# Kernel optimization log

Hardware: AMD Instinct MI355X
Metric: run time of the kernel (lower is better)

The kernel has to match this reference:

```python
import jax, jax.numpy as jnp
import numpy as np

DIM = 768
HEADS = 12
HEAD_DIM = DIM // HEADS
RANK = 8
SCALING = 1.0 / RANK  # lora_alpha / r
SCALE = HEAD_DIM ** -0.5


def setup_inputs() -> dict:
    key = jax.random.key(0)
    ks = jax.random.split(key, 14)
    B, N, D, r = 4, 1024, DIM, RANK
    s = lambda k, shape, sd=0.02: jax.random.normal(k, shape, jnp.float32) * sd
    return {
        "x": jax.random.normal(ks[0], (B, N, D), jnp.float32),
        "qkv_w": s(ks[1], (3 * D, D)),
        "qkv_b": s(ks[2], (3 * D,)),
        "q_base_w": s(ks[3], (D, D)),
        "q_base_b": s(ks[4], (D,)),
        "q_A": s(ks[5], (r, D), 1.0 / r),
        "q_B": s(ks[6], (D, r)),
        "k_base_w": s(ks[7], (D, D)),
        "k_base_b": s(ks[8], (D,)),
        "k_A": s(ks[9], (r, D), 1.0 / r),
        "k_B": s(ks[10], (D, r)),
        "proj_w": s(ks[11], (D, D)),
        "proj_b": s(ks[12], (D,)),
    }


def _lora_linear(x, w, b, A, Bm):
    # base linear + LoRA delta: x@w.T + b + (x@A.T)@B.T * scaling
    return x @ w.T + b + ((x @ A.T) @ Bm.T) * SCALING


def reference(x, qkv_w, qkv_b, q_base_w, q_base_b, q_A, q_B,
              k_base_w, k_base_b, k_A, k_B, proj_w, proj_b):
    B, N, D = x.shape
    H, hd = HEADS, HEAD_DIM
    qkv = (x @ qkv_w.T + qkv_b).reshape(B, N, 3, H, hd).transpose(2, 0, 3, 1, 4)
    q, k, v = qkv[0], qkv[1], qkv[2]  # [B,H,N,hd]
    q_delta = _lora_linear(x, q_base_w, q_base_b, q_A, q_B).reshape(B, N, H, hd).transpose(0, 2, 1, 3)
    k_delta = _lora_linear(x, k_base_w, k_base_b, k_A, k_B).reshape(B, N, H, hd).transpose(0, 2, 1, 3)
    q = q + q_delta
    k = k + k_delta
    attn = jnp.einsum('bhnd,bhmd->bhnm', q, k) * SCALE
    attn = jax.nn.softmax(attn, axis=-1)
    out = jnp.einsum('bhnm,bhmd->bhnd', attn, v)
    out = out.transpose(0, 2, 1, 3).reshape(B, N, D)
    return out @ proj_w.T + proj_b
```

## Files before the change

kernel.cpp:

```cpp
#include <hip/hip_runtime.h>
#include <hip/hip_bf16.h>


typedef _Float16 half8 __attribute__((ext_vector_type(8)));
typedef float f32x4 __attribute__((ext_vector_type(4)));

typedef __attribute__((address_space(3))) unsigned int lds_u32;
typedef __attribute__((address_space(1))) const unsigned int glob_u32;

__device__ __forceinline__ void glds16(const void* g, void* l) {
    __builtin_amdgcn_global_load_lds((glob_u32*)g, (lds_u32*)l, 16, 0, 0);
}

__device__ __forceinline__ float pk2f16(float a, float b) {
    return __builtin_bit_cast(float, __builtin_amdgcn_cvt_pkrtz(a, b));
}

#define SMSCALE 0.18033688011112042f

constexpr size_t OFF_WX = 0;
constexpr size_t OFF_PH = OFF_WX + (size_t)2304*800*2;
constexpr size_t OFF_XE = OFF_PH + (size_t)768*768*2;
constexpr size_t OFF_QH = OFF_XE + (size_t)4096*800*2;
constexpr size_t OFF_KH = OFF_QH + (size_t)48*1024*64*2;
constexpr size_t OFF_VT = OFF_KH + (size_t)48*1024*64*2;
constexpr size_t OFF_AO = OFF_VT + (size_t)48*1024*64*2;

__global__ __launch_bounds__(256)
void pre(const float* __restrict__ qkv_w, const float* __restrict__ qkv_b,
         const float* __restrict__ qw, const float* __restrict__ qbias,
         const float* __restrict__ kw, const float* __restrict__ kbias,
         const float* __restrict__ proj_w, const float* __restrict__ qB,
         const float* __restrict__ kB, const float* __restrict__ x,
         const float* __restrict__ qA, const float* __restrict__ kA,
         _Float16* __restrict__ Wx, _Float16* __restrict__ Ph,
         _Float16* __restrict__ Xe) {
    const int t = threadIdx.x, bb = blockIdx.x;
    if (bb < 2304) {
        const int n = bb;
        const float rs = (n < 768) ? SMSCALE : 1.0f;
        const float* wsrc = qkv_w + (size_t)n * 768;
        const float* fold = (n < 768) ? (qw + (size_t)n * 768)
                          : (n < 1536 ? (kw + (size_t)(n - 768) * 768) : nullptr);
        _Float16* dst = Wx + (size_t)n * 800;
#pragma unroll
        for (int i = 0; i < 3; ++i) {
            const int c = t + i * 256;
            float v = wsrc[c];
            if (fold) v += fold[c];
            dst[c] = (_Float16)(v * rs);
        }
        if (t < 32) {
            float v = 0.f;
            if (t < 8)       { if (n < 768) v = rs * 0.125f * qB[n * 8 + t]; }
            else if (t < 16) { if (n >= 768 && n < 1536) v = 0.125f * kB[(size_t)(n - 768) * 8 + (t - 8)]; }
            else if (t == 16) v = rs * (qkv_b[n] + (n < 768 ? qbias[n] : (n < 1536 ? kbias[n - 768] : 0.f)));
            dst[768 + t] = (_Float16)v;
        }
    } else if (bb < 2880) {
        const size_t idx = ((size_t)(bb - 2304) * 256 + t) * 4;
        const float4 v = *(const float4*)(proj_w + idx);
        _Float16* d = Ph + idx;
        d[0] = (_Float16)v.x; d[1] = (_Float16)v.y;
        d[2] = (_Float16)v.z; d[3] = (_Float16)v.w;
    } else {
        __shared__ float xs[8][768];
        const int m0 = (bb - 2880) * 8;
#pragma unroll
        for (int i = t * 4; i < 6144; i += 1024) {
            const int r = i / 768, c = i - r * 768;
            const float4 v = *(const float4*)(x + (size_t)(m0 + r) * 768 + c);
            xs[r][c] = v.x; xs[r][c + 1] = v.y; xs[r][c + 2] = v.z; xs[r][c + 3] = v.w;
            _Float16* d = Xe + (size_t)(m0 + r) * 800 + c;
            d[0] = (_Float16)v.x; d[1] = (_Float16)v.y; d[2] = (_Float16)v.z; d[3] = (_Float16)v.w;
        }
        __syncthreads();

        const int j = t >> 4, lane = t & 15;
        const float* Arow = (j < 8) ? (qA + (size_t)j * 768) : (kA + (size_t)(j - 8) * 768);
        float accs[8] = {0.f, 0.f, 0.f, 0.f, 0.f, 0.f, 0.f, 0.f};
        for (int k = lane; k < 768; k += 16) {
            const float a = Arow[k];
#pragma unroll
            for (int r = 0; r < 8; ++r) accs[r] += xs[r][k] * a;
        }
#pragma unroll
        for (int r = 0; r < 8; ++r) {
            float acc = accs[r];
            acc += __shfl_xor(acc, 1); acc += __shfl_xor(acc, 2);
            acc += __shfl_xor(acc, 4); acc += __shfl_xor(acc, 8);
            if (lane == 0) Xe[(size_t)(m0 + r) * 800 + 768 + j] = (_Float16)acc;
        }
        if (t < 128) {
            const int r = t >> 4, c = t & 15;
            Xe[(size_t)(m0 + r) * 800 + 784 + c] = (c == 0) ? (_Float16)1.f : (_Float16)0.f;
        }
    }
}

template<int BM, int BN, int MODE>
__global__ __launch_bounds__(256)
void gemm_h(const _Float16* __restrict__ A, const _Float16* __restrict__ Bw,
            const int lda, const int ldb, const int nsteps,
            const float* __restrict__ bias,
            _Float16* __restrict__ Oq, _Float16* __restrict__ Ok, _Float16* __restrict__ Ov,
            float* __restrict__ Co) {
    constexpr int CA = BM / 16, CB = BN / 16, CT = CA + CB;
    constexpr int MI = BM / 32, NI = BN / 32;
    __shared__ __align__(16) _Float16 As[2][BM * 32];
    __shared__ __align__(16) _Float16 Bs[2][BN * 32];
    const int t = threadIdx.x;
    const int w = t >> 6, l = t & 63;
    const int l15 = l & 15, lg = l >> 4;
    const int wm = w >> 1, wn = w & 1;

    const int gx = gridDim.x;
    int lin = blockIdx.y * gx + blockIdx.x;
    lin = (lin & 7) * ((gx * gridDim.y) >> 3) + (lin >> 3);
    const int n0 = (lin % gx) * BN, m0 = (lin / gx) * BM;

    const _Float16* Abase = A + (size_t)(m0 + l15) * lda + lg * 8;
    const _Float16* Bbase = Bw + (size_t)(n0 + l15) * ldb + lg * 8;

    f32x4 acc[MI][NI];
#pragma unroll
    for (int mi = 0; mi < MI; ++mi)
#pragma unroll
        for (int ni = 0; ni < NI; ++ni) acc[mi][ni] = 0.f;

#pragma unroll
    for (int c = w; c < CT; c += 4) {
        if (c < CA) glds16(Abase + (size_t)(c * 16) * lda, &As[0][c * 512]);
        else        glds16(Bbase + (size_t)((c - CA) * 16) * ldb, &Bs[0][(c - CA) * 512]);
    }
    __syncthreads();

    for (int s = 0; s < nsteps; ++s) {
        const int cur = s & 1;
        if (s + 1 < nsteps) {
            const int ko = (s + 1) * 32;
#pragma unroll
            for (int c = w; c < CT; c += 4) {
                if (c < CA) glds16(Abase + (size_t)(c * 16) * lda + ko, &As[cur ^ 1][c * 512]);
                else        glds16(Bbase + (size_t)((c - CA) * 16) * ldb + ko, &Bs[cur ^ 1][(c - CA) * 512]);
            }
        }
        half8 a[MI], b[NI];
#pragma unroll
        for (int mi = 0; mi < MI; ++mi) a[mi] = *(const half8*)&As[cur][(wm * MI + mi) * 512 + l * 8];
#pragma unroll
        for (int ni = 0; ni < NI; ++ni) b[ni] = *(const half8*)&Bs[cur][(wn * NI + ni) * 512 + l * 8];
#pragma unroll
        for (int mi = 0; mi < MI; ++mi)
#pragma unroll
            for (int ni = 0; ni < NI; ++ni)
                acc[mi][ni] = __builtin_amdgcn_mfma_f32_16x16x32_f16(a[mi], b[ni], acc[mi][ni], 0, 0, 0);
        __syncthreads();
    }

    if (MODE == 0) {
        const int sel = (n0 >= 1536) ? 2 : (n0 >= 768 ? 1 : 0);
        const int b_ = m0 >> 10, nnb = m0 & 1023;
        if (sel < 2) {
            _Float16* dst = (sel == 0) ? Oq : Ok;
            const int jb = n0 - sel * 768;
#pragma unroll
            for (int mi = 0; mi < MI; ++mi)
#pragma unroll
                for (int reg = 0; reg < 4; ++reg) {
                    const int nn = nnb + wm * (BM / 2) + mi * 16 + lg * 4 + reg;
#pragma unroll
                    for (int ni = 0; ni < NI; ++ni) {
                        const int jj = jb + wn * (BN / 2) + ni * 16 + l15;
                        const int h = jj >> 6, d = jj & 63;
                        dst[(((size_t)(b_ * 12 + h)) * 1024 + nn) * 64 + d] = (_Float16)acc[mi][ni][reg];
                    }
                }
        } else {
#pragma unroll
            for (int mi = 0; mi < MI; ++mi) {
                const int nn = nnb + wm * (BM / 2) + mi * 16 + lg * 4;
#pragma unroll
                for (int ni = 0; ni < NI; ++ni) {
                    const int jj = (n0 - 1536) + wn * (BN / 2) + ni * 16 + l15;
                    const int h = jj >> 6, d = jj & 63;
                    float2 pv;
                    pv.x = pk2f16(acc[mi][ni][0], acc[mi][ni][1]);
                    pv.y = pk2f16(acc[mi][ni][2], acc[mi][ni][3]);
                    *(float2*)&Ov[(((size_t)(b_ * 12 + h)) * 64 + d) * 1024 + nn] = pv;
                }
            }
        }
    } else {
#pragma unroll
        for (int mi = 0; mi < MI; ++mi)
#pragma unroll
            for (int reg = 0; reg < 4; ++reg) {
                const int m = m0 + wm * (BM / 2) + mi * 16 + lg * 4 + reg;
#pragma unroll
                for (int ni = 0; ni < NI; ++ni) {
                    const int n = n0 + wn * (BN / 2) + ni * 16 + l15;
                    Co[(size_t)m * 768 + n] = acc[mi][ni][reg] + bias[n];
                }
            }
    }
}

#define STAGEK(kbt, buf) { \
_Pragma("unroll") \
    for (int i = 0; i < 4; ++i) { \
        const int c = w * 4 + i; \
        glds16(Kp + (size_t)((kbt) * 64 + (c >> 1) * 16 + l15) * 64 + (c & 1) * 32 + lg * 8, &Ks[buf][c * 512]); \
    } }
#define STAGEV(kbt, buf) { \
_Pragma("unroll") \
    for (int i = 0; i < 4; ++i) { \
        const int c = w * 4 + i; \
        glds16(Vp + (size_t)((c >> 1) * 16 + l15) * 1024 + (kbt) * 64 + (c & 1) * 32 + lg * 8, &Vs[buf][c * 512]); \
    } }
#define QK(buf, s) { \
    half8 kreg[8]; \
_Pragma("unroll") \
    for (int c = 0; c < 8; ++c) kreg[c] = *(const half8*)&Ks[buf][c * 512 + l * 8]; \
_Pragma("unroll") \
    for (int mi = 0; mi < 2; ++mi) \
_Pragma("unroll") \
        for (int nj = 0; nj < 4; ++nj) { \
            s[mi][nj] = 0.f; \
_Pragma("unroll") \
            for (int kh = 0; kh < 2; ++kh) \
                s[mi][nj] = __builtin_amdgcn_mfma_f32_16x16x32_f16(kreg[nj * 2 + kh], qf[mi][kh], s[mi][nj], 0, 0, 0); \
        } }
#define EXPP(ph, s) { \
_Pragma("unroll") \
    for (int mi = 0; mi < 2; ++mi) { \
        float ls = 0.f; \
_Pragma("unroll") \
        for (int nj = 0; nj < 4; ++nj) { \
            const float p0 = __builtin_amdgcn_exp2f(s[mi][nj][0]); \
            const float p1 = __builtin_amdgcn_exp2f(s[mi][nj][1]); \
            const float p2 = __builtin_amdgcn_exp2f(s[mi][nj][2]); \
            const float p3 = __builtin_amdgcn_exp2f(s[mi][nj][3]); \
            ls += (p0 + p1) + (p2 + p3); \
            float2 pk; \
            pk.x = pk2f16(p0, p1); \
            pk.y = pk2f16(p2, p3); \
            const int off = (mi * 2 + (nj >> 1)) * 512 + (2 * (nj & 1) + (lg >> 1)) * 128 \
                          + l15 * 8 + 4 * (lg & 1); \
            *(float2*)&Ps[w][ph][off] = pk; \
        } \
        lsum[mi] += ls; \
    } }
#define PV(ph, buf) { \
    half8 pf[2][2]; \
_Pragma("unroll") \
    for (int mi = 0; mi < 2; ++mi) \
_Pragma("unroll") \
        for (int kh = 0; kh < 2; ++kh) \
            pf[mi][kh] = *(const half8*)&Ps[w][ph][(mi * 2 + kh) * 512 + l * 8]; \
_Pragma("unroll") \
    for (int fj = 0; fj < 4; ++fj) \
_Pragma("unroll") \
        for (int kh = 0; kh < 2; ++kh) { \
            const half8 vf = *(const half8*)&Vs[buf][(fj * 2 + kh) * 512 + l * 8]; \
_Pragma("unroll") \
            for (int mi = 0; mi < 2; ++mi) \
                o[mi][fj] = __builtin_amdgcn_mfma_f32_16x16x32_f16(pf[mi][kh], vf, o[mi][fj], 0, 0, 0); \
        } }

__global__ __launch_bounds__(128)
void attn5(const _Float16* __restrict__ Q, const _Float16* __restrict__ K,
           const _Float16* __restrict__ Vt, _Float16* __restrict__ AO) {
    __shared__ __align__(16) _Float16 Ks[2][4096];
    __shared__ __align__(16) _Float16 Vs[2][4096];
    __shared__ __align__(16) _Float16 Ps[2][2][2048];
    __shared__ float sums[2][32];
    const int t = threadIdx.x;
    const int w = t >> 6, l = t & 63;
    const int l15 = l & 15, lg = l >> 4;

    int lin = blockIdx.y * 16 + blockIdx.x;
    lin = (lin & 7) * 96 + (lin >> 3);
    const int qb = lin & 15, bh = lin >> 4;

    const _Float16* Qp = Q  + (size_t)bh * 65536;
    const _Float16* Kp = K  + (size_t)bh * 65536;
    const _Float16* Vp = Vt + (size_t)bh * 65536;

    STAGEK(0, 0); STAGEK(1, 1); STAGEV(0, 0);
    half8 qf[2][2];
#pragma unroll
    for (int mi = 0; mi < 2; ++mi)
#pragma unroll
        for (int kh = 0; kh < 2; ++kh)
            qf[mi][kh] = *(const half8*)&Qp[(size_t)(qb * 64 + w * 32 + mi * 16 + l15) * 64 + kh * 32 + lg * 8];

    f32x4 o[2][4];
#pragma unroll
    for (int mi = 0; mi < 2; ++mi)
#pragma unroll
        for (int fj = 0; fj < 4; ++fj) o[mi][fj] = 0.f;
    float lsum[2] = {0.f, 0.f};
    __syncthreads();

    {
        f32x4 s[2][4];
        QK(0, s);
        EXPP(0, s);
    }
    __syncthreads();

    for (int kb = 0; kb < 15; ++kb) {
        const int cb = kb & 1, nb = cb ^ 1;
        if (kb + 2 < 16) STAGEK(kb + 2, cb);
        STAGEV(kb + 1, nb);
        f32x4 s[2][4];
        __builtin_amdgcn_s_setprio(1);
        QK(nb, s);
        PV(cb, cb);
        __builtin_amdgcn_s_setprio(0);
        EXPP(nb, s);
        __syncthreads();
    }
    PV(1, 1);

#pragma unroll
    for (int mi = 0; mi < 2; ++mi) {
        float tot = lsum[mi];
        tot += __shfl_xor(tot, 16);
        tot += __shfl_xor(tot, 32);
        if (lg == 0) sums[w][mi * 16 + l15] = tot;
    }
    __builtin_amdgcn_wave_barrier();

    const int b_ = bh / 12, h = bh % 12;
#pragma unroll
    for (int mi = 0; mi < 2; ++mi)
#pragma unroll
        for (int reg = 0; reg < 4; ++reg) {
            const float inv = 1.f / sums[w][mi * 16 + lg * 4 + reg];
            const int tok = qb * 64 + w * 32 + mi * 16 + lg * 4 + reg;
            const size_t base = ((size_t)(b_ * 1024 + tok)) * 768 + h * 64;
#pragma unroll
            for (int fj = 0; fj < 4; ++fj)
                AO[base + fj * 16 + l15] = (_Float16)(o[mi][fj][reg] * inv);
        }
}

extern "C" void kernel_launch(void* const* d_in, const int* in_sizes, int n_in,
                              void* d_out, int out_size, void* d_ws, size_t ws_size,
                              hipStream_t stream) {
    (void)in_sizes; (void)n_in; (void)out_size; (void)ws_size;
    const float* x      = (const float*)d_in[0];
    const float* qkv_w  = (const float*)d_in[1];
    const float* qkv_b  = (const float*)d_in[2];
    const float* q_bw   = (const float*)d_in[3];
    const float* q_bb   = (const float*)d_in[4];
    const float* q_A    = (const float*)d_in[5];
    const float* q_B    = (const float*)d_in[6];
    const float* k_bw   = (const float*)d_in[7];
    const float* k_bb   = (const float*)d_in[8];
    const float* k_A    = (const float*)d_in[9];
    const float* k_B    = (const float*)d_in[10];
    const float* proj_w = (const float*)d_in[11];
    const float* proj_b = (const float*)d_in[12];
    float* out = (float*)d_out;
    char*  ws  = (char*)d_ws;

    _Float16* Wx = (_Float16*)(ws + OFF_WX);
    _Float16* Ph = (_Float16*)(ws + OFF_PH);
    _Float16* Xe = (_Float16*)(ws + OFF_XE);
    _Float16* Qh = (_Float16*)(ws + OFF_QH);
    _Float16* Kh = (_Float16*)(ws + OFF_KH);
    _Float16* Vt = (_Float16*)(ws + OFF_VT);
    _Float16* AO = (_Float16*)(ws + OFF_AO);

    pre<<<dim3(3392), dim3(256), 0, stream>>>(qkv_w, qkv_b, q_bw, q_bb, k_bw, k_bb,
                                              proj_w, q_B, k_B, x, q_A, k_A, Wx, Ph, Xe);
    gemm_h<128, 96, 0><<<dim3(24, 32), dim3(256), 0, stream>>>(
        Xe, Wx, 800, 800, 25, nullptr, Qh, Kh, Vt, nullptr);
    attn5<<<dim3(16, 48), dim3(128), 0, stream>>>(Qh, Kh, Vt, AO);
    gemm_h<64, 96, 1><<<dim3(8, 64), dim3(256), 0, stream>>>(
        AO, Ph, 768, 768, 24, proj_b, nullptr, nullptr, nullptr, out);
}
```

Measured before the change: 99.67 us.

## Restructure attention loop to 128-key tiles with V loaded directly into registers

The attention kernel now processes 128 keys per iteration instead of 64, halving the loop count and the number of barriers. V fragments are read straight from global memory into registers rather than staged through LDS. The software pipeline that overlapped QK of the next tile with PV of the current one is dropped; K is double-buffered in LDS at twice the size. This trades cross-stage overlap and LDS reuse for fewer syncs and less LDS traffic, and it raises register pressure, which the launch bound of one block accepts.

```diff
diff --git a/kernel.cpp b/kernel.cpp
--- a/kernel.cpp
+++ b/kernel.cpp
@@ -206,74 +206,18 @@
     }
 }
 
-#define STAGEK(kbt, buf) { \
+#define STAGEK7(kbt, buf) { \
 _Pragma("unroll") \
-    for (int i = 0; i < 4; ++i) { \
-        const int c = w * 4 + i; \
-        glds16(Kp + (size_t)((kbt) * 64 + (c >> 1) * 16 + l15) * 64 + (c & 1) * 32 + lg * 8, &Ks[buf][c * 512]); \
+    for (int i = 0; i < 8; ++i) { \
+        const int c = w * 8 + i; \
+        glds16(Kp + (size_t)((kbt) * 128 + (c >> 1) * 16 + l15) * 64 + (c & 1) * 32 + lg * 8, &Ks[buf][c * 512]); \
     } }
-#define STAGEV(kbt, buf) { \
-_Pragma("unroll") \
-    for (int i = 0; i < 4; ++i) { \
-        const int c = w * 4 + i; \
-        glds16(Vp + (size_t)((c >> 1) * 16 + l15) * 1024 + (kbt) * 64 + (c & 1) * 32 + lg * 8, &Vs[buf][c * 512]); \
-    } }
-#define QK(buf, s) { \
-    half8 kreg[8]; \
-_Pragma("unroll") \
-    for (int c = 0; c < 8; ++c) kreg[c] = *(const half8*)&Ks[buf][c * 512 + l * 8]; \
-_Pragma("unroll") \
-    for (int mi = 0; mi < 2; ++mi) \
-_Pragma("unroll") \
-        for (int nj = 0; nj < 4; ++nj) { \
-            s[mi][nj] = 0.f; \
-_Pragma("unroll") \
-            for (int kh = 0; kh < 2; ++kh) \
-                s[mi][nj] = __builtin_amdgcn_mfma_f32_16x16x32_f16(kreg[nj * 2 + kh], qf[mi][kh], s[mi][nj], 0, 0, 0); \
-        } }
-#define EXPP(ph, s) { \
-_Pragma("unroll") \
-    for (int mi = 0; mi < 2; ++mi) { \
-        float ls = 0.f; \
-_Pragma("unroll") \
-        for (int nj = 0; nj < 4; ++nj) { \
-            const float p0 = __builtin_amdgcn_exp2f(s[mi][nj][0]); \
-            const float p1 = __builtin_amdgcn_exp2f(s[mi][nj][1]); \
-            const float p2 = __builtin_amdgcn_exp2f(s[mi][nj][2]); \
-            const float p3 = __builtin_amdgcn_exp2f(s[mi][nj][3]); \
-            ls += (p0 + p1) + (p2 + p3); \
-            float2 pk; \
-            pk.x = pk2f16(p0, p1); \
-            pk.y = pk2f16(p2, p3); \
-            const int off = (mi * 2 + (nj >> 1)) * 512 + (2 * (nj & 1) + (lg >> 1)) * 128 \
-                          + l15 * 8 + 4 * (lg & 1); \
-            *(float2*)&Ps[w][ph][off] = pk; \
-        } \
-        lsum[mi] += ls; \
-    } }
-#define PV(ph, buf) { \
-    half8 pf[2][2]; \
-_Pragma("unroll") \
-    for (int mi = 0; mi < 2; ++mi) \
-_Pragma("unroll") \
-        for (int kh = 0; kh < 2; ++kh) \
-            pf[mi][kh] = *(const half8*)&Ps[w][ph][(mi * 2 + kh) * 512 + l * 8]; \
-_Pragma("unroll") \
-    for (int fj = 0; fj < 4; ++fj) \
-_Pragma("unroll") \
-        for (int kh = 0; kh < 2; ++kh) { \
-            const half8 vf = *(const half8*)&Vs[buf][(fj * 2 + kh) * 512 + l * 8]; \
-_Pragma("unroll") \
-            for (int mi = 0; mi < 2; ++mi) \
-                o[mi][fj] = __builtin_amdgcn_mfma_f32_16x16x32_f16(pf[mi][kh], vf, o[mi][fj], 0, 0, 0); \
-        } }
-
-__global__ __launch_bounds__(128)
-void attn5(const _Float16* __restrict__ Q, const _Float16* __restrict__ K,
+
+__global__ __launch_bounds__(128, 1)
+void attn7(const _Float16* __restrict__ Q, const _Float16* __restrict__ K,
            const _Float16* __restrict__ Vt, _Float16* __restrict__ AO) {
-    __shared__ __align__(16) _Float16 Ks[2][4096];
-    __shared__ __align__(16) _Float16 Vs[2][4096];
-    __shared__ __align__(16) _Float16 Ps[2][2][2048];
+    __shared__ __align__(16) _Float16 Ks[2][16384 / 2];
+    __shared__ __align__(16) _Float16 Ps[2][4096];
     __shared__ float sums[2][32];
     const int t = threadIdx.x;
     const int w = t >> 6, l = t & 63;
@@ -287,7 +231,7 @@
     const _Float16* Kp = K  + (size_t)bh * 65536;
     const _Float16* Vp = Vt + (size_t)bh * 65536;
 
-    STAGEK(0, 0); STAGEK(1, 1); STAGEV(0, 0);
+    STAGEK7(0, 0);
     half8 qf[2][2];
 #pragma unroll
     for (int mi = 0; mi < 2; ++mi)
@@ -303,26 +247,68 @@
     float lsum[2] = {0.f, 0.f};
     __syncthreads();
 
-    {
-        f32x4 s[2][4];
-        QK(0, s);
-        EXPP(0, s);
-    }
-    __syncthreads();
-
-    for (int kb = 0; kb < 15; ++kb) {
-        const int cb = kb & 1, nb = cb ^ 1;
-        if (kb + 2 < 16) STAGEK(kb + 2, cb);
-        STAGEV(kb + 1, nb);
-        f32x4 s[2][4];
-        __builtin_amdgcn_s_setprio(1);
-        QK(nb, s);
-        PV(cb, cb);
-        __builtin_amdgcn_s_setprio(0);
-        EXPP(nb, s);
+    for (int kb = 0; kb < 8; ++kb) {
+        const int cur = kb & 1;
+        if (kb < 7) STAGEK7(kb + 1, cur ^ 1);
+
+        half8 vreg[16];
+#pragma unroll
+        for (int fj = 0; fj < 4; ++fj)
+#pragma unroll
+            for (int kh = 0; kh < 4; ++kh)
+                vreg[fj * 4 + kh] = *(const half8*)&Vp[(size_t)(fj * 16 + l15) * 1024
+                                                       + kb * 128 + kh * 32 + lg * 8];
+
+        f32x4 s[2][8];
+#pragma unroll
+        for (int nj = 0; nj < 8; ++nj) {
+            half8 k0 = *(const half8*)&Ks[cur][(nj * 2 + 0) * 512 + l * 8];
+            half8 k1 = *(const half8*)&Ks[cur][(nj * 2 + 1) * 512 + l * 8];
+#pragma unroll
+            for (int mi = 0; mi < 2; ++mi) {
+                f32x4 acc = 0.f;
+                acc = __builtin_amdgcn_mfma_f32_16x16x32_f16(k0, qf[mi][0], acc, 0, 0, 0);
+                acc = __builtin_amdgcn_mfma_f32_16x16x32_f16(k1, qf[mi][1], acc, 0, 0, 0);
+                s[mi][nj] = acc;
+            }
+        }
+
+#pragma unroll
+        for (int mi = 0; mi < 2; ++mi) {
+            float ls = 0.f;
+#pragma unroll
+            for (int nj = 0; nj < 8; ++nj) {
+                const float p0 = __builtin_amdgcn_exp2f(s[mi][nj][0]);
+                const float p1 = __builtin_amdgcn_exp2f(s[mi][nj][1]);
+                const float p2 = __builtin_amdgcn_exp2f(s[mi][nj][2]);
+                const float p3 = __builtin_amdgcn_exp2f(s[mi][nj][3]);
+                ls += (p0 + p1) + (p2 + p3);
+                float2 pk;
+                pk.x = pk2f16(p0, p1);
+                pk.y = pk2f16(p2, p3);
+                const int off = mi * 2048 + (nj >> 1) * 512 + ((nj & 1) * 2 + (lg >> 1)) * 128
+                              + l15 * 8 + (lg & 1) * 4;
+                *(float2*)&Ps[w][off] = pk;
+            }
+            lsum[mi] += ls;
+        }
+
+        half8 pf[2][4];
+#pragma unroll
+        for (int mi = 0; mi < 2; ++mi)
+#pragma unroll
+            for (int kh = 0; kh < 4; ++kh)
+                pf[mi][kh] = *(const half8*)&Ps[w][mi * 2048 + kh * 512 + l * 8];
+#pragma unroll
+        for (int fj = 0; fj < 4; ++fj)
+#pragma unroll
+            for (int kh = 0; kh < 4; ++kh)
+#pragma unroll
+                for (int mi = 0; mi < 2; ++mi)
+                    o[mi][fj] = __builtin_amdgcn_mfma_f32_16x16x32_f16(
+                        pf[mi][kh], vreg[fj * 4 + kh], o[mi][fj], 0, 0, 0);
         __syncthreads();
     }
-    PV(1, 1);
 
 #pragma unroll
     for (int mi = 0; mi < 2; ++mi) {
@@ -379,7 +365,7 @@
                                               proj_w, q_B, k_B, x, q_A, k_A, Wx, Ph, Xe);
     gemm_h<128, 96, 0><<<dim3(24, 32), dim3(256), 0, stream>>>(
         Xe, Wx, 800, 800, 25, nullptr, Qh, Kh, Vt, nullptr);
-    attn5<<<dim3(16, 48), dim3(128), 0, stream>>>(Qh, Kh, Vt, AO);
+    attn7<<<dim3(16, 48), dim3(128), 0, stream>>>(Qh, Kh, Vt, AO);
     gemm_h<64, 96, 1><<<dim3(8, 64), dim3(256), 0, stream>>>(
         AO, Ph, 768, 768, 24, proj_b, nullptr, nullptr, nullptr, out);
 }
```

Result: slower. 106.6 us (+7.0%).
